# Performance work log

Measured on AMD Instinct MI355X. Metric: run time of the kernel, lower is better.

## Reference

```python
import jax, jax.numpy as jnp
import numpy as np

N_NODES = 100000
N_EDGES = 1600000
IN_DIM = 16
HEADS = 4
CH = 32  # per-head channels


def _gat_layer(x, src, dst, W, att_src, att_dst, b, concat):
    """PyG GATConv (eval mode): gather -> edge logits -> segment softmax -> scatter-agg."""
    n = x.shape[0]
    H, C = att_src.shape
    h = (x @ W).reshape(n, H, C)                      # [N,H,C]
    a_src = jnp.einsum('nhc,hc->nh', h, att_src)      # [N,H]
    a_dst = jnp.einsum('nhc,hc->nh', h, att_dst)
    e = jax.nn.leaky_relu(a_src[src] + a_dst[dst], negative_slope=0.2)  # [E,H]
    m = jax.ops.segment_max(e, dst, num_segments=n)   # stable softmax per dst node
    p = jnp.exp(e - m[dst])
    s = jax.ops.segment_sum(p, dst, num_segments=n)
    alpha = p / s[dst]                                 # [E,H]
    out = jax.ops.segment_sum(alpha[:, :, None] * h[src], dst, num_segments=n)  # [N,H,C]
    out = out.reshape(n, H * C) if concat else out.mean(axis=1)
    return out + b


def setup_inputs() -> dict:
    key = jax.random.key(0)
    ks = jax.random.split(key, 20)
    d1 = HEADS * CH  # 128

    def gl(k, shape):  # glorot-ish
        fan = sum(shape[-2:]) if len(shape) > 1 else shape[-1]
        return jax.random.normal(k, shape, dtype=jnp.float32) * (2.0 / fan) ** 0.5

    return {
        'x': jax.random.normal(ks[0], (N_NODES, IN_DIM), dtype=jnp.float32),
        'edge_index': jax.random.randint(ks[1], (2, N_EDGES), 0, N_NODES, dtype=jnp.int32),
        'W1': gl(ks[2], (IN_DIM, d1)), 'aS1': gl(ks[3], (HEADS, CH)), 'aD1': gl(ks[4], (HEADS, CH)), 'b1': jnp.zeros((d1,), jnp.float32),
        'W2': gl(ks[5], (d1, d1)),     'aS2': gl(ks[6], (HEADS, CH)), 'aD2': gl(ks[7], (HEADS, CH)), 'b2': jnp.zeros((d1,), jnp.float32),
        'W3': gl(ks[8], (d1, CH)),     'aS3': gl(ks[9], (1, CH)),     'aD3': gl(ks[10], (1, CH)),    'b3': jnp.zeros((CH,), jnp.float32),
        'reg_w': gl(ks[11], (CH, 1)), 'reg_b': jnp.zeros((1,), jnp.float32),
        'cls_w': gl(ks[12], (CH, 1)), 'cls_b': jnp.zeros((1,), jnp.float32),
    }


def reference(x, edge_index, W1, aS1, aD1, b1, W2, aS2, aD2, b2, W3, aS3, aD3, b3, reg_w, reg_b, cls_w, cls_b):
    n = x.shape[0]
    loops = jnp.arange(n, dtype=edge_index.dtype)  # PyG add_self_loops=True
    src = jnp.concatenate([edge_index[0], loops])
    dst = jnp.concatenate([edge_index[1], loops])

    h = jax.nn.elu(_gat_layer(x, src, dst, W1, aS1, aD1, b1, concat=True))
    h = jax.nn.elu(_gat_layer(h, src, dst, W2, aS2, aD2, b2, concat=True)) + h
    h = jax.nn.elu(_gat_layer(h, src, dst, W3, aS3, aD3, b3, concat=False))

    reg = (h @ reg_w + reg_b).squeeze(-1)
    cls = (h @ cls_w + cls_b).squeeze(-1)
    return reg, cls
```

## Files before the change

### kernel.cpp

```cpp
#include <hip/hip_runtime.h>
#include <hip/hip_bf16.h>
#include <cstdint>

#define CDIV(a,b) (((a)+(b)-1)/(b))

__device__ __forceinline__ float lrelu(float x){ return x > 0.f ? x : 0.2f*x; }
__device__ __forceinline__ float eluf(float x){ return x > 0.f ? x : __expf(x) - 1.f; }
__device__ __forceinline__ unsigned short f2bf(float f){
  unsigned x = __float_as_uint(f);
  return (unsigned short)((x + 0x7fffu + ((x >> 16) & 1u)) >> 16);
}
__device__ __forceinline__ float bf2f(unsigned short u){ return __uint_as_float(((unsigned)u) << 16); }

__global__ void hist_k(const int* __restrict__ ei, int* __restrict__ deg, int ne, int etot){
  int e = blockIdx.x*256 + threadIdx.x;
  if (e >= etot) return;
  int d = (e < ne) ? ei[ne + e] : (e - ne);
  atomicAdd(&deg[d], 1);
}

constexpr int SCHUNK = 2048;

__global__ __launch_bounds__(256) void scan_part_k(const int* __restrict__ in, int* __restrict__ out,
                                                   int* __restrict__ blksum, int n){
  __shared__ int lds[256];
  int base = blockIdx.x*SCHUNK + threadIdx.x*8;
  int v[8]; int tsum = 0;
  #pragma unroll
  for (int k=0;k<8;k++){ int idx=base+k; int x=(idx<n)?in[idx]:0; v[k]=tsum; tsum+=x; }
  lds[threadIdx.x]=tsum; __syncthreads();
  for (int off=1; off<256; off<<=1){
    int y = (threadIdx.x>= (unsigned)off)? lds[threadIdx.x-off]:0;
    __syncthreads();
    lds[threadIdx.x]+=y;
    __syncthreads();
  }
  int excl = lds[threadIdx.x] - tsum;
  #pragma unroll
  for (int k=0;k<8;k++){ int idx=base+k; if(idx<n) out[idx]=excl+v[k]; }
  if (threadIdx.x==255) blksum[blockIdx.x]=lds[255];
}

__global__ __launch_bounds__(256) void scan_top_k(int* __restrict__ blksum, int nb){
  __shared__ int lds[256];
  int x = ((int)threadIdx.x<nb)? blksum[threadIdx.x]:0;
  lds[threadIdx.x]=x; __syncthreads();
  for (int off=1; off<256; off<<=1){
    int y=(threadIdx.x>=(unsigned)off)?lds[threadIdx.x-off]:0;
    __syncthreads();
    lds[threadIdx.x]+=y;
    __syncthreads();
  }
  if ((int)threadIdx.x<nb) blksum[threadIdx.x]=lds[threadIdx.x]-x;
}

__global__ void scan_add_k(int* __restrict__ rowstart, const int* __restrict__ blksum,
                           int* __restrict__ cursor, int n, int etot){
  int i = blockIdx.x*256+threadIdx.x;
  if (i<n){ int r = rowstart[i]+blksum[i/SCHUNK]; rowstart[i]=r; cursor[i]=r; }
  if (i==0) rowstart[n]=etot;
}

__global__ void scatter_k(const int* __restrict__ ei, int* __restrict__ cursor,
                          int* __restrict__ edge_src, int ne, int etot, int lo, int hi){
  int e = blockIdx.x*256+threadIdx.x;
  if (e>=etot) return;
  int s,d;
  if (e<ne){ s=ei[e]; d=ei[ne+e]; } else { s=e-ne; d=s; }
  if (d < lo || d >= hi) return;
  int p = atomicAdd(&cursor[d],1);
  edge_src[p]=s;
}

template<int K, int KC, int M, int NPT, int H>
__global__ __launch_bounds__(256) void gemm_att_k(const float* __restrict__ X, const float* __restrict__ W,
    const float* __restrict__ attS, const float* __restrict__ attD,
    unsigned short* __restrict__ Hb, float* __restrict__ asrc, float* __restrict__ adst, int n){
  constexpr int CG = M/8;
  constexpr int NG = 256/CG;
  constexpr int NT = NG*NPT;
  constexpr int XS = KC + 4;
  __shared__ float Xl[NT*XS];
  __shared__ float Wl[KC*M];

  const int tid = threadIdx.x;
  const int cg  = tid % CG;
  const int nd  = tid / CG;
  const int base = blockIdx.x * NT;

  float acc[NPT][8];
  #pragma unroll
  for (int j=0;j<NPT;++j)
    #pragma unroll
    for (int c=0;c<8;++c) acc[j][c]=0.f;

  for (int kc0 = 0; kc0 < K; kc0 += KC){
    __syncthreads();
    for (int i = tid; i < NT*KC/4; i += 256){
      int node = i / (KC/4);
      int k4   = i % (KC/4);
      float4 v = make_float4(0.f,0.f,0.f,0.f);
      if (base + node < n) v = *(const float4*)&X[(size_t)(base+node)*K + kc0 + k4*4];
      *(float4*)&Xl[node*XS + k4*4] = v;
    }
    const float* Wsrc = W + (size_t)kc0*M;
    for (int i = tid; i < KC*M/4; i += 256)
      *(float4*)&Wl[i*4] = *(const float4*)&Wsrc[i*4];
    __syncthreads();

    #pragma unroll 4
    for (int k4 = 0; k4 < KC/4; ++k4){
      float4 xv[NPT];
      #pragma unroll
      for (int j=0;j<NPT;++j) xv[j] = *(const float4*)&Xl[(nd + NG*j)*XS + k4*4];
      #pragma unroll
      for (int kk=0;kk<4;++kk){
        float4 w0 = *(const float4*)&Wl[(k4*4+kk)*M + cg*8];
        float4 w1 = *(const float4*)&Wl[(k4*4+kk)*M + cg*8 + 4];
        #pragma unroll
        for (int j=0;j<NPT;++j){
          float x = ((const float*)&xv[j])[kk];
          acc[j][0] += x*w0.x; acc[j][1] += x*w0.y; acc[j][2] += x*w0.z; acc[j][3] += x*w0.w;
          acc[j][4] += x*w1.x; acc[j][5] += x*w1.y; acc[j][6] += x*w1.z; acc[j][7] += x*w1.w;
        }
      }
    }
  }

  const int c0 = cg*8;
  float s0=attS[c0],s1=attS[c0+1],s2=attS[c0+2],s3=attS[c0+3],
        s4=attS[c0+4],s5=attS[c0+5],s6=attS[c0+6],s7=attS[c0+7];
  float d0=attD[c0],d1=attD[c0+1],d2=attD[c0+2],d3=attD[c0+3],
        d4=attD[c0+4],d5=attD[c0+5],d6=attD[c0+6],d7=attD[c0+7];
  #pragma unroll
  for (int j=0;j<NPT;++j){
    int node = base + nd + NG*j;
    float vs = acc[j][0]*s0+acc[j][1]*s1+acc[j][2]*s2+acc[j][3]*s3
             + acc[j][4]*s4+acc[j][5]*s5+acc[j][6]*s6+acc[j][7]*s7;
    float vd = acc[j][0]*d0+acc[j][1]*d1+acc[j][2]*d2+acc[j][3]*d3
             + acc[j][4]*d4+acc[j][5]*d5+acc[j][6]*d6+acc[j][7]*d7;
    vs += __shfl_xor(vs,1); vs += __shfl_xor(vs,2);
    vd += __shfl_xor(vd,1); vd += __shfl_xor(vd,2);
    if (node < n){
      uint4 pk;
      pk.x = (unsigned)f2bf(acc[j][0]) | ((unsigned)f2bf(acc[j][1])<<16);
      pk.y = (unsigned)f2bf(acc[j][2]) | ((unsigned)f2bf(acc[j][3])<<16);
      pk.z = (unsigned)f2bf(acc[j][4]) | ((unsigned)f2bf(acc[j][5])<<16);
      pk.w = (unsigned)f2bf(acc[j][6]) | ((unsigned)f2bf(acc[j][7])<<16);
      *(uint4*)&Hb[(size_t)node*M + c0] = pk;
      if ((cg & 3)==0){
        int head = cg>>2;
        asrc[(size_t)node*H+head]=vs;
        adst[(size_t)node*H+head]=vd;
      }
    }
  }
}

template<bool RES>
__global__ __launch_bounds__(256) void agg4_k(const unsigned short* __restrict__ Hb, const float* __restrict__ asrc,
    const float* __restrict__ adst, const int* __restrict__ rowstart, const int* __restrict__ esrc,
    const float* __restrict__ bias, float* __restrict__ out, int n){
  __shared__ float alphaS[4][64][4];
  const int w    = threadIdx.x >> 6;
  const int lane = threadIdx.x & 63;
  int wid  = (int)((blockIdx.x*256 + threadIdx.x) >> 6);
  if (wid >= n) return;
  wid = __builtin_amdgcn_readfirstlane(wid);
  const int rs = rowstart[wid], re = rowstart[wid+1];
  const int deg = re - rs;
  const float4 adv = *(const float4*)&adst[(size_t)wid*4];
  const int head = lane >> 4;

  float acc0 = 0.f, acc1 = 0.f;

  if (deg <= 64){
    int s = 0;
    float l0=-1e30f,l1=-1e30f,l2=-1e30f,l3=-1e30f;
    if (lane < deg){
      s = esrc[rs + lane];
      float4 a4 = *(const float4*)&asrc[(size_t)s*4];
      l0 = lrelu(a4.x+adv.x); l1 = lrelu(a4.y+adv.y);
      l2 = lrelu(a4.z+adv.z); l3 = lrelu(a4.w+adv.w);
    }
    float m0=l0,m1=l1,m2=l2,m3=l3;
    #pragma unroll
    for (int mask=32; mask; mask>>=1){
      m0=fmaxf(m0,__shfl_xor(m0,mask)); m1=fmaxf(m1,__shfl_xor(m1,mask));
      m2=fmaxf(m2,__shfl_xor(m2,mask)); m3=fmaxf(m3,__shfl_xor(m3,mask));
    }
    float e0=__expf(l0-m0), e1=__expf(l1-m1), e2=__expf(l2-m2), e3=__expf(l3-m3);
    float s0=e0,s1=e1,s2=e2,s3=e3;
    #pragma unroll
    for (int mask=32; mask; mask>>=1){
      s0+=__shfl_xor(s0,mask); s1+=__shfl_xor(s1,mask);
      s2+=__shfl_xor(s2,mask); s3+=__shfl_xor(s3,mask);
    }
    *(float4*)&alphaS[w][lane][0] = make_float4(e0/s0, e1/s1, e2/s2, e3/s3);

    int jj = 0;
    for (; jj+8 <= deg; jj += 8){
      int sj0 = __builtin_amdgcn_readlane(s, jj+0);
      int sj1 = __builtin_amdgcn_readlane(s, jj+1);
      int sj2 = __builtin_amdgcn_readlane(s, jj+2);
      int sj3 = __builtin_amdgcn_readlane(s, jj+3);
      int sj4 = __builtin_amdgcn_readlane(s, jj+4);
      int sj5 = __builtin_amdgcn_readlane(s, jj+5);
      int sj6 = __builtin_amdgcn_readlane(s, jj+6);
      int sj7 = __builtin_amdgcn_readlane(s, jj+7);
      ushort2 h0 = ((const ushort2*)(Hb + (size_t)sj0*128))[lane];
      ushort2 h1 = ((const ushort2*)(Hb + (size_t)sj1*128))[lane];
      ushort2 h2 = ((const ushort2*)(Hb + (size_t)sj2*128))[lane];
      ushort2 h3 = ((const ushort2*)(Hb + (size_t)sj3*128))[lane];
      ushort2 h4 = ((const ushort2*)(Hb + (size_t)sj4*128))[lane];
      ushort2 h5 = ((const ushort2*)(Hb + (size_t)sj5*128))[lane];
      ushort2 h6 = ((const ushort2*)(Hb + (size_t)sj6*128))[lane];
      ushort2 h7 = ((const ushort2*)(Hb + (size_t)sj7*128))[lane];
      float a0 = alphaS[w][jj+0][head];
      float a1 = alphaS[w][jj+1][head];
      float a2 = alphaS[w][jj+2][head];
      float a3 = alphaS[w][jj+3][head];
      float a4 = alphaS[w][jj+4][head];
      float a5 = alphaS[w][jj+5][head];
      float a6 = alphaS[w][jj+6][head];
      float a7 = alphaS[w][jj+7][head];
      acc0 += a0*bf2f(h0.x) + a1*bf2f(h1.x) + a2*bf2f(h2.x) + a3*bf2f(h3.x)
            + a4*bf2f(h4.x) + a5*bf2f(h5.x) + a6*bf2f(h6.x) + a7*bf2f(h7.x);
      acc1 += a0*bf2f(h0.y) + a1*bf2f(h1.y) + a2*bf2f(h2.y) + a3*bf2f(h3.y)
            + a4*bf2f(h4.y) + a5*bf2f(h5.y) + a6*bf2f(h6.y) + a7*bf2f(h7.y);
    }
    for (; jj+4 <= deg; jj += 4){
      int sj0 = __builtin_amdgcn_readlane(s, jj+0);
      int sj1 = __builtin_amdgcn_readlane(s, jj+1);
      int sj2 = __builtin_amdgcn_readlane(s, jj+2);
      int sj3 = __builtin_amdgcn_readlane(s, jj+3);
      ushort2 h0 = ((const ushort2*)(Hb + (size_t)sj0*128))[lane];
      ushort2 h1 = ((const ushort2*)(Hb + (size_t)sj1*128))[lane];
      ushort2 h2 = ((const ushort2*)(Hb + (size_t)sj2*128))[lane];
      ushort2 h3 = ((const ushort2*)(Hb + (size_t)sj3*128))[lane];
      float a0 = alphaS[w][jj+0][head];
      float a1 = alphaS[w][jj+1][head];
      float a2 = alphaS[w][jj+2][head];
      float a3 = alphaS[w][jj+3][head];
      acc0 += a0*bf2f(h0.x) + a1*bf2f(h1.x) + a2*bf2f(h2.x) + a3*bf2f(h3.x);
      acc1 += a0*bf2f(h0.y) + a1*bf2f(h1.y) + a2*bf2f(h2.y) + a3*bf2f(h3.y);
    }
    for (; jj < deg; ++jj){
      int sj = __builtin_amdgcn_readlane(s, jj);
      ushort2 hv = ((const ushort2*)(Hb + (size_t)sj*128))[lane];
      float a = alphaS[w][jj][head];
      acc0 += a*bf2f(hv.x);
      acc1 += a*bf2f(hv.y);
    }
  } else {
    float adl[4] = {adv.x, adv.y, adv.z, adv.w};
    float m[4] = {-1e30f,-1e30f,-1e30f,-1e30f};
    for (int i = rs + lane; i < re; i += 64){
      int s = esrc[i];
      float4 a4 = *(const float4*)&asrc[(size_t)s*4];
      m[0]=fmaxf(m[0], lrelu(a4.x+adl[0]));
      m[1]=fmaxf(m[1], lrelu(a4.y+adl[1]));
      m[2]=fmaxf(m[2], lrelu(a4.z+adl[2]));
      m[3]=fmaxf(m[3], lrelu(a4.w+adl[3]));
    }
    #pragma unroll
    for (int h=0; h<4; ++h){
      #pragma unroll
      for (int mask=32; mask; mask>>=1) m[h] = fmaxf(m[h], __shfl_xor(m[h], mask));
    }
    float sum[4] = {0.f,0.f,0.f,0.f};
    for (int i = rs + lane; i < re; i += 64){
      int s = esrc[i];
      float4 a4 = *(const float4*)&asrc[(size_t)s*4];
      sum[0]+=__expf(lrelu(a4.x+adl[0])-m[0]);
      sum[1]+=__expf(lrelu(a4.y+adl[1])-m[1]);
      sum[2]+=__expf(lrelu(a4.z+adl[2])-m[2]);
      sum[3]+=__expf(lrelu(a4.w+adl[3])-m[3]);
    }
    #pragma unroll
    for (int h=0; h<4; ++h){
      #pragma unroll
      for (int mask=32; mask; mask>>=1) sum[h]+=__shfl_xor(sum[h],mask);
    }
    const float ad = adl[head], mm = m[head], iv = 1.f/sum[head];
    int i = rs;
    for (; i+4 <= re; i += 4){
      int s0=esrc[i], s1=esrc[i+1], s2=esrc[i+2], s3=esrc[i+3];
      float a0 = asrc[(size_t)s0*4+head];
      float a1 = asrc[(size_t)s1*4+head];
      float a2 = asrc[(size_t)s2*4+head];
      float a3 = asrc[(size_t)s3*4+head];
      ushort2 h0 = ((const ushort2*)(Hb + (size_t)s0*128))[lane];
      ushort2 h1 = ((const ushort2*)(Hb + (size_t)s1*128))[lane];
      ushort2 h2 = ((const ushort2*)(Hb + (size_t)s2*128))[lane];
      ushort2 h3 = ((const ushort2*)(Hb + (size_t)s3*128))[lane];
      float e0=__expf(lrelu(a0+ad)-mm)*iv;
      float e1=__expf(lrelu(a1+ad)-mm)*iv;
      float e2=__expf(lrelu(a2+ad)-mm)*iv;
      float e3=__expf(lrelu(a3+ad)-mm)*iv;
      acc0 += e0*bf2f(h0.x) + e1*bf2f(h1.x) + e2*bf2f(h2.x) + e3*bf2f(h3.x);
      acc1 += e0*bf2f(h0.y) + e1*bf2f(h1.y) + e2*bf2f(h2.y) + e3*bf2f(h3.y);
    }
    for (; i < re; ++i){
      int s = esrc[i];
      float a = asrc[(size_t)s*4+head];
      ushort2 hv = ((const ushort2*)(Hb + (size_t)s*128))[lane];
      float e = __expf(lrelu(a+ad)-mm)*iv;
      acc0 += e*bf2f(hv.x);
      acc1 += e*bf2f(hv.y);
    }
  }

  float2 bv = *(const float2*)&bias[2*lane];
  float v0 = eluf(acc0 + bv.x);
  float v1 = eluf(acc1 + bv.y);
  if (RES){
    float2 rv = *(const float2*)&out[(size_t)wid*128 + 2*lane];
    v0 += rv.x; v1 += rv.y;
  }
  *(float2*)&out[(size_t)wid*128 + 2*lane] = make_float2(v0, v1);
}

__global__ __launch_bounds__(256) void agg1_heads_k(const unsigned short* __restrict__ Hb, const float* __restrict__ asrc,
    const float* __restrict__ adst, const int* __restrict__ rowstart, const int* __restrict__ esrc,
    const float* __restrict__ bias,
    const float* __restrict__ rw, const float* __restrict__ rb,
    const float* __restrict__ cw, const float* __restrict__ cb,
    float* __restrict__ out, int n){
  __shared__ float alphaS[4][64];
  const int w    = threadIdx.x >> 6;
  const int lane = threadIdx.x & 63;
  int wid  = (int)((blockIdx.x*256 + threadIdx.x) >> 6);
  if (wid >= n) return;
  wid = __builtin_amdgcn_readfirstlane(wid);
  const int rs = rowstart[wid], re = rowstart[wid+1];
  const int deg = re - rs;
  const float adl = adst[wid];
  const int q = lane >> 4, c2 = lane & 15;

  float acc0 = 0.f, acc1 = 0.f;

  if (deg <= 64){
    int s = 0;
    float l = -1e30f;
    if (lane < deg){
      s = esrc[rs + lane];
      l = lrelu(asrc[s]+adl);
    }
    float m = l;
    #pragma unroll
    for (int mask=32; mask; mask>>=1) m = fmaxf(m, __shfl_xor(m, mask));
    float e = __expf(l-m);
    float sum = e;
    #pragma unroll
    for (int mask=32; mask; mask>>=1) sum += __shfl_xor(sum, mask);
    alphaS[w][lane] = e/sum;

    for (int jj = 0; jj < deg; jj += 4){
      int idx = jj + q;
      int sj = __shfl(s, idx);
      float av = (idx < 64) ? alphaS[w][idx] : 0.f;
      ushort2 hv = ((const ushort2*)(Hb + (size_t)sj*32))[c2];
      acc0 += av*bf2f(hv.x);
      acc1 += av*bf2f(hv.y);
    }
  } else {
    float m = -1e30f;
    for (int i = rs + lane; i < re; i += 64) m = fmaxf(m, lrelu(asrc[esrc[i]]+adl));
    #pragma unroll
    for (int mask=32; mask; mask>>=1) m = fmaxf(m, __shfl_xor(m, mask));
    float sum = 0.f;
    for (int i = rs + lane; i < re; i += 64) sum += __expf(lrelu(asrc[esrc[i]]+adl)-m);
    #pragma unroll
    for (int mask=32; mask; mask>>=1) sum += __shfl_xor(sum, mask);
    const float iv = 1.f/sum;
    for (int i = rs; i < re; i += 4){
      int eidx = i + q;
      if (eidx < re){
        int s = esrc[eidx];
        float a = asrc[s];
        float e = __expf(lrelu(a+adl)-m)*iv;
        ushort2 hv = ((const ushort2*)(Hb + (size_t)s*32))[c2];
        acc0 += e*bf2f(hv.x);
        acc1 += e*bf2f(hv.y);
      }
    }
  }

  acc0 += __shfl_xor(acc0,16); acc0 += __shfl_xor(acc0,32);
  acc1 += __shfl_xor(acc1,16); acc1 += __shfl_xor(acc1,32);

  float2 bv = *(const float2*)&bias[2*c2];
  float v0 = eluf(acc0 + bv.x);
  float v1 = eluf(acc1 + bv.y);
  float r  = v0*rw[2*c2] + v1*rw[2*c2+1];
  float cl = v0*cw[2*c2] + v1*cw[2*c2+1];
  #pragma unroll
  for (int mask=1; mask<16; mask<<=1){ r += __shfl_xor(r, mask); cl += __shfl_xor(cl, mask); }
  if (lane == 0){
    out[wid]     = r  + rb[0];
    out[n + wid] = cl + cb[0];
  }
}

extern "C" void kernel_launch(void* const* d_in, const int* in_sizes, int n_in,
                              void* d_out, int out_size, void* d_ws, size_t ws_size,
                              hipStream_t stream){
  const float* x   = (const float*)d_in[0];
  const int*   ei  = (const int*)d_in[1];
  const float* W1  = (const float*)d_in[2];
  const float* aS1 = (const float*)d_in[3];
  const float* aD1 = (const float*)d_in[4];
  const float* b1  = (const float*)d_in[5];
  const float* W2  = (const float*)d_in[6];
  const float* aS2 = (const float*)d_in[7];
  const float* aD2 = (const float*)d_in[8];
  const float* b2  = (const float*)d_in[9];
  const float* W3  = (const float*)d_in[10];
  const float* aS3 = (const float*)d_in[11];
  const float* aD3 = (const float*)d_in[12];
  const float* b3  = (const float*)d_in[13];
  const float* rw  = (const float*)d_in[14];
  const float* rb  = (const float*)d_in[15];
  const float* cw  = (const float*)d_in[16];
  const float* cb  = (const float*)d_in[17];
  float* out = (float*)d_out;

  const int n    = in_sizes[0] / 16;
  const int ne   = in_sizes[1] / 2;
  const int etot = ne + n;

  float* A    = (float*)d_ws;
  float* Bf   = A  + (size_t)n*128;
  unsigned short* Hb = (unsigned short*)Bf;
  float* asrc = Bf + (size_t)n*128;
  float* adst = asrc + (size_t)n*4;
  int* deg    = (int*)(adst + (size_t)n*4);
  int* rowst  = deg + n;
  int* cursor = rowst + n + 1;
  int* esrc   = cursor + n;
  int* blksum = esrc + etot;

  hipMemsetAsync(deg, 0, (size_t)n*sizeof(int), stream);
  hist_k<<<CDIV(etot,256),256,0,stream>>>(ei, deg, ne, etot);
  int nblk = CDIV(n, SCHUNK);
  scan_part_k<<<nblk,256,0,stream>>>(deg, rowst, blksum, n);
  scan_top_k<<<1,256,0,stream>>>(blksum, nblk);
  scan_add_k<<<CDIV(n,256),256,0,stream>>>(rowst, blksum, cursor, n, etot);
  for (int p = 0; p < 4; ++p){
    int lo = (int)((size_t)n * p / 4);
    int hi = (int)((size_t)n * (p+1) / 4);
    scatter_k<<<CDIV(etot,256),256,0,stream>>>(ei, cursor, esrc, ne, etot, lo, hi);
  }

  gemm_att_k<16,16,128,4,4><<<CDIV(n,64),256,0,stream>>>(x, W1, aS1, aD1, Hb, asrc, adst, n);
  agg4_k<false><<<CDIV(n,4),256,0,stream>>>(Hb, asrc, adst, rowst, esrc, b1, A, n);

  gemm_att_k<128,32,128,4,4><<<CDIV(n,64),256,0,stream>>>(A, W2, aS2, aD2, Hb, asrc, adst, n);
  agg4_k<true><<<CDIV(n,4),256,0,stream>>>(Hb, asrc, adst, rowst, esrc, b2, A, n);

  gemm_att_k<128,32,32,1,1><<<CDIV(n,64),256,0,stream>>>(A, W3, aS3, aD3, Hb, asrc, adst, n);
  agg1_heads_k<<<CDIV(n,4),256,0,stream>>>(Hb, asrc, adst, rowst, esrc, b3, rw, rb, cw, cb, out, n);
}
```

Baseline: 580.7 us.

## Fuse CSR build into a single cooperative kernel with grid syncs

After: 1.975 ms. 240% more time.

```diff
diff --git a/kernel.cpp b/kernel.cpp
--- a/kernel.cpp
+++ b/kernel.cpp
@@ -1,6 +1,9 @@
 #include <hip/hip_runtime.h>
 #include <hip/hip_bf16.h>
+#include <hip/hip_cooperative_groups.h>
 #include <cstdint>
+
+namespace cg = cooperative_groups;
 
 #define CDIV(a,b) (((a)+(b)-1)/(b))
 
@@ -12,64 +15,78 @@
 }
 __device__ __forceinline__ float bf2f(unsigned short u){ return __uint_as_float(((unsigned)u) << 16); }
 
-__global__ void hist_k(const int* __restrict__ ei, int* __restrict__ deg, int ne, int etot){
-  int e = blockIdx.x*256 + threadIdx.x;
-  if (e >= etot) return;
-  int d = (e < ne) ? ei[ne + e] : (e - ne);
-  atomicAdd(&deg[d], 1);
-}
-
 constexpr int SCHUNK = 2048;
 
-__global__ __launch_bounds__(256) void scan_part_k(const int* __restrict__ in, int* __restrict__ out,
-                                                   int* __restrict__ blksum, int n){
+__global__ __launch_bounds__(256) void csr_build_k(const int* __restrict__ ei,
+    int* __restrict__ deg, int* __restrict__ rowst, int* __restrict__ cursor,
+    int* __restrict__ esrc, int* __restrict__ blksum, int n, int ne, int etot){
+  cg::grid_group grid = cg::this_grid();
   __shared__ int lds[256];
-  int base = blockIdx.x*SCHUNK + threadIdx.x*8;
-  int v[8]; int tsum = 0;
-  #pragma unroll
-  for (int k=0;k<8;k++){ int idx=base+k; int x=(idx<n)?in[idx]:0; v[k]=tsum; tsum+=x; }
-  lds[threadIdx.x]=tsum; __syncthreads();
-  for (int off=1; off<256; off<<=1){
-    int y = (threadIdx.x>= (unsigned)off)? lds[threadIdx.x-off]:0;
-    __syncthreads();
-    lds[threadIdx.x]+=y;
-    __syncthreads();
-  }
-  int excl = lds[threadIdx.x] - tsum;
-  #pragma unroll
-  for (int k=0;k<8;k++){ int idx=base+k; if(idx<n) out[idx]=excl+v[k]; }
-  if (threadIdx.x==255) blksum[blockIdx.x]=lds[255];
-}
-
-__global__ __launch_bounds__(256) void scan_top_k(int* __restrict__ blksum, int nb){
-  __shared__ int lds[256];
-  int x = ((int)threadIdx.x<nb)? blksum[threadIdx.x]:0;
-  lds[threadIdx.x]=x; __syncthreads();
-  for (int off=1; off<256; off<<=1){
-    int y=(threadIdx.x>=(unsigned)off)?lds[threadIdx.x-off]:0;
-    __syncthreads();
-    lds[threadIdx.x]+=y;
-    __syncthreads();
-  }
-  if ((int)threadIdx.x<nb) blksum[threadIdx.x]=lds[threadIdx.x]-x;
-}
-
-__global__ void scan_add_k(int* __restrict__ rowstart, const int* __restrict__ blksum,
-                           int* __restrict__ cursor, int n, int etot){
-  int i = blockIdx.x*256+threadIdx.x;
-  if (i<n){ int r = rowstart[i]+blksum[i/SCHUNK]; rowstart[i]=r; cursor[i]=r; }
-  if (i==0) rowstart[n]=etot;
-}
-
-__global__ void scatter_k(const int* __restrict__ ei, int* __restrict__ cursor,
-                          int* __restrict__ edge_src, int ne, int etot, int lo, int hi){
-  int e = blockIdx.x*256+threadIdx.x;
-  if (e>=etot) return;
-  int s,d;
-  if (e<ne){ s=ei[e]; d=ei[ne+e]; } else { s=e-ne; d=s; }
-  if (d < lo || d >= hi) return;
-  int p = atomicAdd(&cursor[d],1);
-  edge_src[p]=s;
+  const int tid = blockIdx.x*256 + threadIdx.x;
+  const int gsz = gridDim.x*256;
+
+  for (int i = tid; i < n; i += gsz) deg[i] = 0;
+  grid.sync();
+
+  for (int e = tid; e < etot; e += gsz){
+    int d = (e < ne) ? ei[ne + e] : (e - ne);
+    atomicAdd(&deg[d], 1);
+  }
+  grid.sync();
+
+  const int nblk = CDIV(n, SCHUNK);
+  if ((int)blockIdx.x < nblk){
+    int base = blockIdx.x*SCHUNK + threadIdx.x*8;
+    int v[8]; int tsum = 0;
+    #pragma unroll
+    for (int k=0;k<8;k++){ int idx=base+k; int x=(idx<n)?deg[idx]:0; v[k]=tsum; tsum+=x; }
+    lds[threadIdx.x]=tsum; __syncthreads();
+    for (int off=1; off<256; off<<=1){
+      int y = (threadIdx.x>= (unsigned)off)? lds[threadIdx.x-off]:0;
+      __syncthreads();
+      lds[threadIdx.x]+=y;
+      __syncthreads();
+    }
+    int excl = lds[threadIdx.x] - tsum;
+    #pragma unroll
+    for (int k=0;k<8;k++){ int idx=base+k; if(idx<n) rowst[idx]=excl+v[k]; }
+    if (threadIdx.x==255) blksum[blockIdx.x]=lds[255];
+  }
+  grid.sync();
+
+  if (blockIdx.x == 0){
+    int x = ((int)threadIdx.x<nblk)? blksum[threadIdx.x]:0;
+    lds[threadIdx.x]=x; __syncthreads();
+    for (int off=1; off<256; off<<=1){
+      int y=(threadIdx.x>=(unsigned)off)?lds[threadIdx.x-off]:0;
+      __syncthreads();
+      lds[threadIdx.x]+=y;
+      __syncthreads();
+    }
+    if ((int)threadIdx.x<nblk) blksum[threadIdx.x]=lds[threadIdx.x]-x;
+  }
+  grid.sync();
+
+  for (int i = tid; i < n; i += gsz){
+    int r = rowst[i] + blksum[i/SCHUNK];
+    rowst[i] = r; cursor[i] = r;
+  }
+  if (tid == 0) rowst[n] = etot;
+  grid.sync();
+
+  for (int wdw = 0; wdw < 4; ++wdw){
+    int lo = (int)((long long)n * wdw / 4);
+    int hi = (int)((long long)n * (wdw+1) / 4);
+    for (int e = tid; e < etot; e += gsz){
+      int s,d;
+      if (e<ne){ s=ei[e]; d=ei[ne+e]; } else { s=e-ne; d=s; }
+      if (d >= lo && d < hi){
+        int p = atomicAdd(&cursor[d],1);
+        esrc[p]=s;
+      }
+    }
+    grid.sync();
+  }
 }
 
 template<int K, int KC, int M, int NPT, int H>
@@ -441,16 +458,13 @@
   int* esrc   = cursor + n;
   int* blksum = esrc + etot;
 
-  hipMemsetAsync(deg, 0, (size_t)n*sizeof(int), stream);
-  hist_k<<<CDIV(etot,256),256,0,stream>>>(ei, deg, ne, etot);
-  int nblk = CDIV(n, SCHUNK);
-  scan_part_k<<<nblk,256,0,stream>>>(deg, rowst, blksum, n);
-  scan_top_k<<<1,256,0,stream>>>(blksum, nblk);
-  scan_add_k<<<CDIV(n,256),256,0,stream>>>(rowst, blksum, cursor, n, etot);
-  for (int p = 0; p < 4; ++p){
-    int lo = (int)((size_t)n * p / 4);
-    int hi = (int)((size_t)n * (p+1) / 4);
-    scatter_k<<<CDIV(etot,256),256,0,stream>>>(ei, cursor, esrc, ne, etot, lo, hi);
+  {
+    const int* ei_a = ei; int* deg_a = deg; int* rowst_a = rowst; int* cursor_a = cursor;
+    int* esrc_a = esrc; int* blksum_a = blksum;
+    int n_a = n, ne_a = ne, etot_a = etot;
+    void* args[] = { (void*)&ei_a, (void*)&deg_a, (void*)&rowst_a, (void*)&cursor_a,
+                     (void*)&esrc_a, (void*)&blksum_a, (void*)&n_a, (void*)&ne_a, (void*)&etot_a };
+    hipLaunchCooperativeKernel((void*)csr_build_k, dim3(1536), dim3(256), args, 0, stream);
   }
 
   gemm_att_k<16,16,128,4,4><<<CDIV(n,64),256,0,stream>>>(x, W1, aS1, aD1, Hb, asrc, adst, n);
```
